# Kernel optimization log

Hardware: AMD Instinct MI355X
Metric: run time of the kernel (lower is better)

Reference implementation:

```python
import jax, jax.numpy as jnp
import numpy as np

D_MODEL, HEAD_DIM = 1024, 128

def setup_inputs() -> dict:
    key = jax.random.key(0)
    kx, kq, kk, kv = jax.random.split(key, 4)
    x = jax.random.normal(kx, (4, 4096, D_MODEL), dtype=jnp.float32)
    s = 1.0 / np.sqrt(D_MODEL)
    Wq = jax.random.normal(kq, (D_MODEL, HEAD_DIM), dtype=jnp.float32) * s
    Wk = jax.random.normal(kk, (D_MODEL, HEAD_DIM), dtype=jnp.float32) * s
    Wv = jax.random.normal(kv, (D_MODEL, HEAD_DIM), dtype=jnp.float32) * s
    return {"x": x, "Wq": Wq, "Wk": Wk, "Wv": Wv}

def reference(x, Wq, Wk, Wv):
    # x: [b, s, d_model]; Wq/Wk/Wv: [d_model, head_dim]
    q = jnp.einsum('bsd,dh->bsh', x, Wq)
    k = jnp.einsum('bsd,dh->bsh', x, Wk)
    v = jnp.einsum('bsd,dh->bsh', x, Wv)
    seq = x.shape[1]
    scale = 1.0 / jnp.sqrt(jnp.asarray(q.shape[-1], q.dtype))
    scores = jnp.einsum('bqh,bkh->bqk', q, k) * scale  # [b, s, s]
    causal = jnp.tril(jnp.ones((seq, seq), dtype=bool))
    scores = jnp.where(causal, scores, jnp.asarray(-jnp.inf, scores.dtype))
    attn = jax.nn.softmax(scores, axis=-1)
    return jnp.einsum('bqk,bkh->bqh', attn, v)
```

## Files before the change

kernel.cpp:

```cpp
#include <hip/hip_runtime.h>
#include <hip/hip_bf16.h>
#include <math.h>

#define D_MODEL 1024
#define HD 128
#define SEQ 4096

typedef __bf16 bf16x8 __attribute__((ext_vector_type(8)));
typedef float f32x4 __attribute__((ext_vector_type(4)));
typedef unsigned int u32;
typedef u32 u32x4 __attribute__((ext_vector_type(4)));

__device__ __forceinline__ unsigned short f2bf(float f) {
    union { float f; u32 u; } c; c.f = f;
    u32 u = c.u;
    u = (u + 0x7fffu + ((u >> 16) & 1u)) >> 16;
    return (unsigned short)u;
}
__device__ __forceinline__ u32 pk2(float a, float b) {
    __hip_bfloat162 h = __float22bfloat162_rn(make_float2(a, b));
    union { __hip_bfloat162 h; u32 u; } c; c.h = h; return c.u;
}
__device__ __forceinline__ void dma16(void* lds, const void* g) {
    __builtin_amdgcn_global_load_lds(
        (const __attribute__((address_space(1))) u32*)g,
        (__attribute__((address_space(3))) u32*)lds, 16, 0, 0);
}
__device__ __forceinline__ void drain_dma()  { __builtin_amdgcn_s_waitcnt(0x0F70); }

__global__ __launch_bounds__(256)
void wt_kernel(const float* __restrict__ Wq, const float* __restrict__ Wk,
               const float* __restrict__ Wv, unsigned short* __restrict__ Wt) {
    __shared__ float wsf[64][129];
    const int t = threadIdx.x;
    const int k0 = blockIdx.x * 64;
    const int mat = blockIdx.y;
    const float* W = (mat == 0) ? Wq : (mat == 1) ? Wk : Wv;
    const float sc = (mat == 0) ? (0.08838834764831845f * 1.4426950408889634f) : 1.0f;
    {
        const int r = t >> 2, c = (t & 3) * 32;
        const float* src = W + (size_t)(k0 + r) * HD + c;
        #pragma unroll
        for (int j = 0; j < 32; j += 4)
            *reinterpret_cast<f32x4*>(&wsf[r][c + j]) = *reinterpret_cast<const f32x4*>(src + j);
    }
    __syncthreads();
    const int n = t >> 1, ks = (t & 1) * 32;
    u32 ow[16];
    #pragma unroll
    for (int j = 0; j < 16; ++j)
        ow[j] = pk2(wsf[ks + 2 * j][n] * sc, wsf[ks + 2 * j + 1][n] * sc);
    unsigned short* dst = Wt + (size_t)(mat * HD + n) * D_MODEL + k0 + ks;
    #pragma unroll
    for (int j = 0; j < 4; ++j)
        *reinterpret_cast<u32x4*>(dst + j * 8) = (u32x4){ow[4*j], ow[4*j+1], ow[4*j+2], ow[4*j+3]};
}

__global__ __launch_bounds__(512, 2)
void proj_kernel(const float* __restrict__ x, const unsigned short* __restrict__ Wt,
                 unsigned short* __restrict__ Qb, unsigned short* __restrict__ Kb,
                 unsigned short* __restrict__ Vt) {
    __shared__ __align__(1024) char ps[131072];
    const int t = threadIdx.x;
    const int w = t >> 6, l = t & 63, li = l & 15, g2 = l >> 4;
    const int mh = w >> 2, nq = w & 3;
    const int rowbase = blockIdx.x * 64;

    const int lr = l >> 3, lg = l & 7;
    const int cg = lg ^ lr;
    const int wn_add = (cg >> 2) * 192;
    const int wkq = (cg & 3) * 8;

    auto stage = [&](int it) {
        const int k0 = it * 32;
        const int buf = it & 3;
        dma16(ps + buf * 8192 + w * 1024,
              x + (size_t)(rowbase + w * 8 + lr) * D_MODEL + k0 + cg * 4);
        #pragma unroll
        for (int j = 0; j < 3; ++j) {
            int r0 = w * 24 + j * 8;
            dma16(ps + 32768 + buf * 24576 + r0 * 128,
                  Wt + (size_t)(r0 + lr + wn_add) * D_MODEL + k0 + wkq);
        }
    };

    f32x4 acc[2][6];
    #pragma unroll
    for (int mt = 0; mt < 2; ++mt)
        #pragma unroll
        for (int nt = 0; nt < 6; ++nt) acc[mt][nt] = (f32x4){0.f, 0.f, 0.f, 0.f};

    stage(0); stage(1); stage(2);
    for (int it = 0; it < 32; ++it) {
        if (it < 30)       asm volatile("s_waitcnt vmcnt(8) lgkmcnt(0)" ::: "memory");
        else if (it == 30) asm volatile("s_waitcnt vmcnt(4) lgkmcnt(0)" ::: "memory");
        else               asm volatile("s_waitcnt vmcnt(0) lgkmcnt(0)" ::: "memory");
        __builtin_amdgcn_s_barrier();
        if (it + 3 < 32) stage(it + 3);

        const char* xb = ps + (it & 3) * 8192;
        const char* wb = ps + 32768 + (it & 3) * 24576;

        bf16x8 bf[6];
        #pragma unroll
        for (int nt = 0; nt < 6; ++nt) {
            int r = (nq & 1) * 96 + nt * 16 + li;
            bf[nt] = *reinterpret_cast<const bf16x8*>(
                wb + r * 128 + ((((nq >> 1) * 4 + g2) ^ (li & 7)) * 16));
        }
        __builtin_amdgcn_s_setprio(1);
        #pragma unroll
        for (int mt = 0; mt < 2; ++mt) {
            int row = mh * 32 + mt * 16 + li;
            int p0 = ((2 * g2) ^ (li & 7)) * 16;
            f32x4 x0 = *reinterpret_cast<const f32x4*>(xb + row * 128 + p0);
            f32x4 x1 = *reinterpret_cast<const f32x4*>(xb + row * 128 + (p0 ^ 16));
            union { u32 d[4]; bf16x8 v; } cva;
            cva.d[0] = pk2(x0[0], x0[1]); cva.d[1] = pk2(x0[2], x0[3]);
            cva.d[2] = pk2(x1[0], x1[1]); cva.d[3] = pk2(x1[2], x1[3]);
            bf16x8 af = cva.v;
            #pragma unroll
            for (int nt = 0; nt < 6; ++nt)
                acc[mt][nt] = __builtin_amdgcn_mfma_f32_16x16x32_bf16(af, bf[nt], acc[mt][nt], 0, 0, 0);
        }
        __builtin_amdgcn_s_setprio(0);
    }

    #pragma unroll
    for (int nt = 0; nt < 6; ++nt) {
        const int c0 = nq * 96 + nt * 16;
        #pragma unroll
        for (int mt = 0; mt < 2; ++mt) {
            const int m0 = mh * 32 + mt * 16 + g2 * 4;
            if (c0 < 256) {
                unsigned short* P = (c0 < 128) ? Qb : Kb;
                const int col = (c0 < 128 ? c0 : c0 - 128) + li;
                #pragma unroll
                for (int r = 0; r < 4; ++r)
                    P[(size_t)(rowbase + m0 + r) * HD + col] = f2bf(acc[mt][nt][r]);
            } else {
                const int d = c0 - 256 + li;
                const int b_ = rowbase >> 12, s_ = (rowbase + m0) & 4095;
                ushort4 s4;
                s4.x = f2bf(acc[mt][nt][0]); s4.y = f2bf(acc[mt][nt][1]);
                s4.z = f2bf(acc[mt][nt][2]); s4.w = f2bf(acc[mt][nt][3]);
                *reinterpret_cast<ushort4*>(&Vt[((size_t)b_ * HD + d) * SEQ + s_]) = s4;
            }
        }
    }
}

__global__ __launch_bounds__(256, 2)
void attn_kernel(const unsigned short* __restrict__ Qb, const unsigned short* __restrict__ Kb,
                 const unsigned short* __restrict__ Vt, float* __restrict__ outO,
                 unsigned short* __restrict__ Obf, float* __restrict__ Lbuf) {
    __shared__ __align__(1024) char smem[73728];
    const int t = threadIdx.x;
    const int w = t >> 6, l = t & 63, li = l & 15, g2 = l >> 4;
    const int qh = w >> 1, kh = w & 1;
    const int b = blockIdx.x & 3;
    const int u = blockIdx.x >> 2;
    const int g = 63 - (u >> 2);
    const int c = u & 3;
    const int R = g + 1;
    const int ts = (c * R) >> 2, te = ((c + 1) * R) >> 2;
    const int q0 = g * 64;
    const size_t rowb = (size_t)b * SEQ;
    const int koff = kh * 32;

    const unsigned short* KbB = Kb + rowb * HD;
    const unsigned short* VtB = Vt + (size_t)b * HD * SEQ;
    const int vgran = ((l & 7) ^ (l >> 3)) * 8;

    auto stage = [&](int it, char* base) {
        const int j0 = it * 64;
        #pragma unroll
        for (int j = 0; j < 4; ++j) {
            int rK = w * 16 + 4 * j + (l >> 4);
            dma16(base + (w * 16 + 4 * j) * 256,
                  KbB + (size_t)(j0 + rK) * 128 + (((l & 15) ^ (rK & 7)) * 8));
            int rV = w * 32 + 8 * j + (l >> 3);
            dma16(base + 16384 + (w * 32 + 8 * j) * 128,
                  VtB + (size_t)rV * SEQ + j0 + vgran);
        }
    };

    bf16x8 qf[2][4];
    #pragma unroll
    for (int qt = 0; qt < 2; ++qt)
        #pragma unroll
        for (int ks = 0; ks < 4; ++ks)
            qf[qt][ks] = *reinterpret_cast<const bf16x8*>(
                Qb + (rowb + q0 + qh * 32 + qt * 16 + li) * HD + ks * 32 + g2 * 8);

    f32x4 acco[2][8];
    #pragma unroll
    for (int qt = 0; qt < 2; ++qt)
        #pragma unroll
        for (int dt = 0; dt < 8; ++dt) acco[qt][dt] = (f32x4){0.f, 0.f, 0.f, 0.f};
    float ls[2] = {0.f, 0.f};

    const int gV = ((4 * kh + g2) ^ (li & 7)) * 16;

    if (ts < te) stage(ts, smem);
    for (int it = ts; it < te; ++it) {
        char* cbuf = smem + ((it - ts) & 1) * 32768;
        char* nbuf = smem + (((it - ts) & 1) ^ 1) * 32768;
        drain_dma();
        __syncthreads();
        if (it + 1 < te) stage(it + 1, nbuf);

        f32x4 accs[2][2];
        #pragma unroll
        for (int qt = 0; qt < 2; ++qt)
            #pragma unroll
            for (int kt = 0; kt < 2; ++kt) accs[qt][kt] = (f32x4){0.f, 0.f, 0.f, 0.f};
        #pragma unroll
        for (int kt = 0; kt < 2; ++kt) {
            const char* kb = cbuf + (koff + kt * 16 + li) * 256;
            #pragma unroll
            for (int ks = 0; ks < 4; ++ks) {
                bf16x8 kf = *reinterpret_cast<const bf16x8*>(kb + (((4 * ks + g2) ^ (li & 7)) * 16));
                accs[0][kt] = __builtin_amdgcn_mfma_f32_16x16x32_bf16(kf, qf[0][ks], accs[0][kt], 0, 0, 0);
                accs[1][kt] = __builtin_amdgcn_mfma_f32_16x16x32_bf16(kf, qf[1][ks], accs[1][kt], 0, 0, 0);
            }
        }

        const bool masked = (it == g);
        #pragma unroll
        for (int qt = 0; qt < 2; ++qt) {
            const int prow = qh * 32 + qt * 16 + li;
            #pragma unroll
            for (int kt = 0; kt < 2; ++kt) {
                float p[4];
                #pragma unroll
                for (int r = 0; r < 4; ++r) {
                    float s = accs[qt][kt][r];
                    if (masked && (koff + kt * 16 + g2 * 4 + r > prow)) s = -INFINITY;
                    p[r] = __builtin_amdgcn_exp2f(s - 16.0f);
                    ls[qt] += p[r];
                }
                union { u32 d[2]; uint2 v; } pw;
                pw.d[0] = pk2(p[0], p[1]); pw.d[1] = pk2(p[2], p[3]);
                int gr = (kh * 4 + kt * 2 + (g2 >> 1)) ^ (prow & 7);
                *reinterpret_cast<uint2*>(
                    smem + 65536 + prow * 128 + gr * 16 + (g2 & 1) * 8) = pw.v;
            }
        }

        bf16x8 pb[2];
        #pragma unroll
        for (int qt = 0; qt < 2; ++qt) {
            const int prow = qh * 32 + qt * 16 + li;
            pb[qt] = *reinterpret_cast<const bf16x8*>(
                smem + 65536 + prow * 128 + (((kh * 4 + g2) ^ (prow & 7)) * 16));
        }
        #pragma unroll
        for (int dt = 0; dt < 8; ++dt) {
            bf16x8 va = *reinterpret_cast<const bf16x8*>(cbuf + 16384 + (dt * 16 + li) * 128 + gV);
            acco[0][dt] = __builtin_amdgcn_mfma_f32_16x16x32_bf16(va, pb[0], acco[0][dt], 0, 0, 0);
            acco[1][dt] = __builtin_amdgcn_mfma_f32_16x16x32_bf16(va, pb[1], acco[1][dt], 0, 0, 0);
        }
    }

    #pragma unroll
    for (int qt = 0; qt < 2; ++qt) {
        ls[qt] += __shfl_xor(ls[qt], 16);
        ls[qt] += __shfl_xor(ls[qt], 32);
    }

    float (*Osum)[132] = (float(*)[132])smem;
    float* Lsh = (float*)(smem + 33792);
    __syncthreads();
    if (l < 16) {
        Lsh[kh * 64 + qh * 32 + l]      = ls[0];
        Lsh[kh * 64 + qh * 32 + 16 + l] = ls[1];
    }
    if (kh == 0) {
        #pragma unroll
        for (int qt = 0; qt < 2; ++qt)
            #pragma unroll
            for (int dt = 0; dt < 8; ++dt)
                *reinterpret_cast<f32x4*>(
                    &Osum[qh * 32 + qt * 16 + li][dt * 16 + g2 * 4]) = acco[qt][dt];
    }
    __syncthreads();
    if (kh == 1) {
        #pragma unroll
        for (int qt = 0; qt < 2; ++qt)
            #pragma unroll
            for (int dt = 0; dt < 8; ++dt) {
                f32x4* p = reinterpret_cast<f32x4*>(
                    &Osum[qh * 32 + qt * 16 + li][dt * 16 + g2 * 4]);
                f32x4 v = *p;
                #pragma unroll
                for (int j = 0; j < 4; ++j) v[j] += acco[qt][dt][j];
                *p = v;
            }
    }
    __syncthreads();

    if (t < 64)
        Lbuf[(size_t)c * 16384 + rowb + q0 + t] = Lsh[t] + Lsh[64 + t];
    #pragma unroll
    for (int k = 0; k < 8; ++k) {
        int idx = t + k * 256;
        int row = idx >> 5, col = (idx & 31) * 4;
        f32x4 o = *reinterpret_cast<const f32x4*>(&Osum[row][col]);
        size_t grow = rowb + q0 + row;
        if (c == 3) {
            *reinterpret_cast<f32x4*>(&outO[grow * HD + col]) = o;
        } else {
            union { u32 d[2]; uint2 v; } pkd;
            pkd.d[0] = pk2(o[0], o[1]); pkd.d[1] = pk2(o[2], o[3]);
            *reinterpret_cast<uint2*>(&Obf[(size_t)c * 2097152 + grow * HD + col]) = pkd.v;
        }
    }
}

__global__ __launch_bounds__(256)
void merge_kernel(float* __restrict__ outO, const unsigned short* __restrict__ Obf,
                  const float* __restrict__ Lbuf) {
    int tid = blockIdx.x * 256 + threadIdx.x;
    #pragma unroll
    for (int k = 0; k < 4; ++k) {
        int idx = tid + k * 131072;
        int row = idx >> 5, col = (idx & 31) * 4;
        float lsum = Lbuf[row] + Lbuf[16384 + row] + Lbuf[32768 + row] + Lbuf[49152 + row];
        float inv = 1.f / lsum;
        f32x4 o = *reinterpret_cast<const f32x4*>(&outO[(size_t)row * HD + col]);
        #pragma unroll
        for (int cc = 0; cc < 3; ++cc) {
            ushort4 uu = *reinterpret_cast<const ushort4*>(
                &Obf[(size_t)cc * 2097152 + (size_t)row * HD + col]);
            union { u32 u; float f; } a, b2, c2, d2;
            a.u = (u32)uu.x << 16; b2.u = (u32)uu.y << 16;
            c2.u = (u32)uu.z << 16; d2.u = (u32)uu.w << 16;
            o[0] += a.f; o[1] += b2.f; o[2] += c2.f; o[3] += d2.f;
        }
        #pragma unroll
        for (int j = 0; j < 4; ++j) o[j] *= inv;
        *reinterpret_cast<f32x4*>(&outO[(size_t)row * HD + col]) = o;
    }
}

extern "C" void kernel_launch(void* const* d_in, const int* in_sizes, int n_in,
                              void* d_out, int out_size, void* d_ws, size_t ws_size,
                              hipStream_t stream) {
    const float* x  = (const float*)d_in[0];
    const float* Wq = (const float*)d_in[1];
    const float* Wk = (const float*)d_in[2];
    const float* Wv = (const float*)d_in[3];
    float* out = (float*)d_out;

    char* ws = (char*)d_ws;
    unsigned short* Qb  = (unsigned short*)(ws);
    unsigned short* Kb  = (unsigned short*)(ws + ((size_t)4  << 20));
    unsigned short* Vt  = (unsigned short*)(ws + ((size_t)8  << 20));
    unsigned short* Wt  = (unsigned short*)(ws + ((size_t)12 << 20));
    unsigned short* Obf = (unsigned short*)(ws + ((size_t)13 << 20));
    float*          Lb  = (float*)(ws + ((size_t)25 << 20));

    wt_kernel   <<<dim3(16, 3), dim3(256), 0, stream>>>(Wq, Wk, Wv, Wt);
    proj_kernel <<<dim3(256),   dim3(512), 0, stream>>>(x, Wt, Qb, Kb, Vt);
    attn_kernel <<<dim3(1024),  dim3(256), 0, stream>>>(Qb, Kb, Vt, out, Obf, Lb);
    merge_kernel<<<dim3(512),   dim3(256), 0, stream>>>(out, Obf, Lb);
}
```

Before: 168.5 us.

## Double projection block to 1024 threads with one M-tile per wave

The projection kernel now runs 16 waves per block instead of 8, and each wave computes a single 16-row M tile instead of two. The DMA staging work is redistributed across the waves, the wait counts are lowered to match, and s_setprio is removed. The aim is more waves to hide latency and fewer accumulators per wave. The cost is one block per CU at launch bounds 1024, and each wave repeats the B-fragment LDS reads for half the MFMA work.

```diff
diff --git a/kernel.cpp b/kernel.cpp
--- a/kernel.cpp
+++ b/kernel.cpp
@@ -56,7 +56,7 @@
         *reinterpret_cast<u32x4*>(dst + j * 8) = (u32x4){ow[4*j], ow[4*j+1], ow[4*j+2], ow[4*j+3]};
 }
 
-__global__ __launch_bounds__(512, 2)
+__global__ __launch_bounds__(1024, 1)
 void proj_kernel(const float* __restrict__ x, const unsigned short* __restrict__ Wt,
                  unsigned short* __restrict__ Qb, unsigned short* __restrict__ Kb,
                  unsigned short* __restrict__ Vt) {
@@ -74,26 +74,30 @@
     auto stage = [&](int it) {
         const int k0 = it * 32;
         const int buf = it & 3;
-        dma16(ps + buf * 8192 + w * 1024,
-              x + (size_t)(rowbase + w * 8 + lr) * D_MODEL + k0 + cg * 4);
-        #pragma unroll
-        for (int j = 0; j < 3; ++j) {
-            int r0 = w * 24 + j * 8;
-            dma16(ps + 32768 + buf * 24576 + r0 * 128,
-                  Wt + (size_t)(r0 + lr + wn_add) * D_MODEL + k0 + wkq);
+        char* xb = ps + buf * 8192;
+        char* wbuf = ps + 32768 + buf * 24576;
+        if (w < 8) {
+            dma16(xb + w * 1024,
+                  x + (size_t)(rowbase + w * 8 + lr) * D_MODEL + k0 + cg * 4);
+            dma16(wbuf + w * 1024,
+                  Wt + (size_t)(w * 8 + lr + wn_add) * D_MODEL + k0 + wkq);
+        } else {
+            const int j0 = 8 + (w - 8) * 2;
+            dma16(wbuf + j0 * 1024,
+                  Wt + (size_t)(j0 * 8 + lr + wn_add) * D_MODEL + k0 + wkq);
+            dma16(wbuf + (j0 + 1) * 1024,
+                  Wt + (size_t)((j0 + 1) * 8 + lr + wn_add) * D_MODEL + k0 + wkq);
         }
     };
 
-    f32x4 acc[2][6];
-    #pragma unroll
-    for (int mt = 0; mt < 2; ++mt)
-        #pragma unroll
-        for (int nt = 0; nt < 6; ++nt) acc[mt][nt] = (f32x4){0.f, 0.f, 0.f, 0.f};
+    f32x4 acc[6];
+    #pragma unroll
+    for (int nt = 0; nt < 6; ++nt) acc[nt] = (f32x4){0.f, 0.f, 0.f, 0.f};
 
     stage(0); stage(1); stage(2);
     for (int it = 0; it < 32; ++it) {
-        if (it < 30)       asm volatile("s_waitcnt vmcnt(8) lgkmcnt(0)" ::: "memory");
-        else if (it == 30) asm volatile("s_waitcnt vmcnt(4) lgkmcnt(0)" ::: "memory");
+        if (it < 30)       asm volatile("s_waitcnt vmcnt(4) lgkmcnt(0)" ::: "memory");
+        else if (it == 30) asm volatile("s_waitcnt vmcnt(2) lgkmcnt(0)" ::: "memory");
         else               asm volatile("s_waitcnt vmcnt(0) lgkmcnt(0)" ::: "memory");
         __builtin_amdgcn_s_barrier();
         if (it + 3 < 32) stage(it + 3);
@@ -108,10 +112,8 @@
             bf[nt] = *reinterpret_cast<const bf16x8*>(
                 wb + r * 128 + ((((nq >> 1) * 4 + g2) ^ (li & 7)) * 16));
         }
-        __builtin_amdgcn_s_setprio(1);
-        #pragma unroll
-        for (int mt = 0; mt < 2; ++mt) {
-            int row = mh * 32 + mt * 16 + li;
+        {
+            int row = mh * 16 + li;
             int p0 = ((2 * g2) ^ (li & 7)) * 16;
             f32x4 x0 = *reinterpret_cast<const f32x4*>(xb + row * 128 + p0);
             f32x4 x1 = *reinterpret_cast<const f32x4*>(xb + row * 128 + (p0 ^ 16));
@@ -121,31 +123,27 @@
             bf16x8 af = cva.v;
             #pragma unroll
             for (int nt = 0; nt < 6; ++nt)
-                acc[mt][nt] = __builtin_amdgcn_mfma_f32_16x16x32_bf16(af, bf[nt], acc[mt][nt], 0, 0, 0);
-        }
-        __builtin_amdgcn_s_setprio(0);
+                acc[nt] = __builtin_amdgcn_mfma_f32_16x16x32_bf16(af, bf[nt], acc[nt], 0, 0, 0);
+        }
     }
 
     #pragma unroll
     for (int nt = 0; nt < 6; ++nt) {
         const int c0 = nq * 96 + nt * 16;
-        #pragma unroll
-        for (int mt = 0; mt < 2; ++mt) {
-            const int m0 = mh * 32 + mt * 16 + g2 * 4;
-            if (c0 < 256) {
-                unsigned short* P = (c0 < 128) ? Qb : Kb;
-                const int col = (c0 < 128 ? c0 : c0 - 128) + li;
-                #pragma unroll
-                for (int r = 0; r < 4; ++r)
-                    P[(size_t)(rowbase + m0 + r) * HD + col] = f2bf(acc[mt][nt][r]);
-            } else {
-                const int d = c0 - 256 + li;
-                const int b_ = rowbase >> 12, s_ = (rowbase + m0) & 4095;
-                ushort4 s4;
-                s4.x = f2bf(acc[mt][nt][0]); s4.y = f2bf(acc[mt][nt][1]);
-                s4.z = f2bf(acc[mt][nt][2]); s4.w = f2bf(acc[mt][nt][3]);
-                *reinterpret_cast<ushort4*>(&Vt[((size_t)b_ * HD + d) * SEQ + s_]) = s4;
-            }
+        const int m0 = rowbase + mh * 16 + g2 * 4;
+        if (c0 < 256) {
+            unsigned short* P = (c0 < 128) ? Qb : Kb;
+            const int col = (c0 < 128 ? c0 : c0 - 128) + li;
+            #pragma unroll
+            for (int r = 0; r < 4; ++r)
+                P[(size_t)(m0 + r) * HD + col] = f2bf(acc[nt][r]);
+        } else {
+            const int d = c0 - 256 + li;
+            const int b_ = m0 >> 12, s_ = m0 & 4095;
+            ushort4 s4;
+            s4.x = f2bf(acc[nt][0]); s4.y = f2bf(acc[nt][1]);
+            s4.z = f2bf(acc[nt][2]); s4.w = f2bf(acc[nt][3]);
+            *reinterpret_cast<ushort4*>(&Vt[((size_t)b_ * HD + d) * SEQ + s_]) = s4;
         }
     }
 }
@@ -362,7 +360,7 @@
     float*          Lb  = (float*)(ws + ((size_t)25 << 20));
 
     wt_kernel   <<<dim3(16, 3), dim3(256), 0, stream>>>(Wq, Wk, Wv, Wt);
-    proj_kernel <<<dim3(256),   dim3(512), 0, stream>>>(x, Wt, Qb, Kb, Vt);
+    proj_kernel <<<dim3(256),   dim3(1024), 0, stream>>>(x, Wt, Qb, Kb, Vt);
     attn_kernel <<<dim3(1024),  dim3(256), 0, stream>>>(Qb, Kb, Vt, out, Obf, Lb);
     merge_kernel<<<dim3(512),   dim3(256), 0, stream>>>(out, Obf, Lb);
 }
```

Measured after the change: 165.9 us. No clear change (-1.5%).
